# Kernel optimization log

Hardware: AMD Instinct MI355X
Metric: run time of the kernel (lower is better)

## Reference

```python
import jax, jax.numpy as jnp
import numpy as np

N, E, F_IN, F_OUT = 50000, 1600000, 256, 64
ALPHA = 0.2  # LeakyReLU negative slope


def setup_inputs() -> dict:
    key = jax.random.key(0)
    k1, k2, k3, k4 = jax.random.split(key, 4)
    x = jax.random.normal(k1, (N, F_IN), dtype=jnp.float32)
    edge = jax.random.randint(k2, (2, E), 0, N)  # COO (row, col) indices of adj
    # xavier_normal with gain=1.414 (as in the torch module)
    W = jax.random.normal(k3, (F_IN, F_OUT), dtype=jnp.float32) * (1.414 * np.sqrt(2.0 / (F_IN + F_OUT)))
    a = jax.random.normal(k4, (1, 2 * F_OUT), dtype=jnp.float32) * (1.414 * np.sqrt(2.0 / (1 + 2 * F_OUT)))
    return {"x": x, "edge": edge, "W": W, "a": a}


def reference(x, edge, W, a):
    # eval mode: dropout is a no-op
    Wh = x @ W  # [N, F_OUT]
    src, dst = edge[0], edge[1]
    # a @ concat(Wh[src], Wh[dst]) per edge, computed as two node-level dots then gathered
    s_src = Wh @ a[0, :F_OUT]   # [N]
    s_dst = Wh @ a[0, F_OUT:]   # [N]
    score = s_src[src] + s_dst[dst]                      # [E]
    edge_e = jnp.exp(-jax.nn.leaky_relu(score, ALPHA))   # [E]
    # sparse-softmax denominator: row sums of exp scores
    e_rowsum = jax.ops.segment_sum(edge_e, src, num_segments=N)  # [N]
    # weighted aggregation: h_prime[i] = sum_{(i,j) in E} e_ij * Wh[j]
    h_prime = jax.ops.segment_sum(edge_e[:, None] * Wh[dst], src, num_segments=N)  # [N, F_OUT]
    h_prime = h_prime / e_rowsum[:, None]
    return jax.nn.elu(h_prime)  # concat=True -> ELU
```

## Files before the change

### kernel.cpp

```cpp
#include <hip/hip_runtime.h>
#include <hip/hip_fp16.h>

#define N_NODES 50000
#define N_EDGES 1600000
#define F_IN 256
#define F_OUT 64
#define ALPHA 0.2f

#define BS 64
#define NBK 782
#define NSUB 8
#define CAP 384
#define EB 2048
#define NBB 782
#define LDS_CAP 4096
#define OF_CAP 16384

typedef __attribute__((ext_vector_type(8))) short bf16x8;
typedef __attribute__((ext_vector_type(4))) float f32x4;

__device__ inline unsigned short f2bf(float f) {
    unsigned int u = __float_as_uint(f);
    return (unsigned short)((u + 0x7FFFu + ((u >> 16) & 1u)) >> 16);
}
__device__ inline float bf2f(unsigned short b) {
    return __uint_as_float(((unsigned int)b) << 16);
}

__device__ inline void fmix_lo(float& a, unsigned int u, float s) {
    asm("v_fma_mix_f32 %0, %1, %2, %0 op_sel:[0,0,0] op_sel_hi:[1,0,0]"
        : "+v"(a) : "v"(u), "v"(s));
}
__device__ inline void fmix_hi(float& a, unsigned int u, float s) {
    asm("v_fma_mix_f32 %0, %1, %2, %0 op_sel:[1,0,0] op_sel_hi:[1,0,0]"
        : "+v"(a) : "v"(u), "v"(s));
}

__global__ __launch_bounds__(256) void gat_wprep(
    const float* __restrict__ W, unsigned short* __restrict__ Wf,
    int* __restrict__ cnt, int* __restrict__ of_cnt)
{
    const int di = blockIdx.x * 256 + threadIdx.x;
    if (di < NSUB * NBK) cnt[di] = 0;
    if (di == 0) of_cnt[0] = 0;
    const int j    = di & 7;
    const int lane = (di >> 3) & 63;
    const int tile = di >> 9;
    const int ks   = tile >> 2;
    const int nt   = tile & 3;
    const int k = ks * 32 + (lane >> 4) * 8 + j;
    const int n = nt * 16 + (lane & 15);
    Wf[di] = f2bf(W[k * F_OUT + n]);
}

__global__ __launch_bounds__(256) void gat_fused(
    const float* __restrict__ x, const unsigned short* __restrict__ Wf,
    const float* __restrict__ a, unsigned short* __restrict__ Whh,
    float* __restrict__ s_src, float* __restrict__ s_dst,
    const int* __restrict__ edge, int* __restrict__ cnt,
    unsigned int* __restrict__ arr, int* __restrict__ of_cnt,
    int2* __restrict__ of_list)
{
    __shared__ __align__(16) unsigned char smem[32768];
    const int t = threadIdx.x;

    if (blockIdx.x >= NBB) {
        unsigned short* Wl = (unsigned short*)smem;
        {
            const float4* __restrict__ src = (const float4*)Wf;
            float4* dst = (float4*)Wl;
            #pragma unroll
            for (int i = 0; i < 8; ++i) dst[t + i * 256] = src[t + i * 256];
        }
        __syncthreads();

        const int lane = t & 63;
        const int w    = t >> 6;
        const int q    = lane >> 4;
        const int c16  = lane & 15;
        const bf16x8* __restrict__ Wfrag = (const bf16x8*)Wl;

        float av[4], av2[4];
        #pragma unroll
        for (int nt = 0; nt < 4; ++nt) {
            av[nt]  = a[nt * 16 + c16];
            av2[nt] = a[F_OUT + nt * 16 + c16];
        }

        const int c = blockIdx.x - NBB;
        const int node0 = c * 64 + w * 16;
        int row = node0 + c16;
        if (row >= N_NODES) row = N_NODES - 1;
        const float4* __restrict__ xp = (const float4*)(x + (size_t)row * F_IN);

        float4 xv[16];
        #pragma unroll
        for (int ks = 0; ks < 8; ++ks) {
            xv[2 * ks]     = xp[ks * 8 + q * 2];
            xv[2 * ks + 1] = xp[ks * 8 + q * 2 + 1];
        }

        f32x4 acc[4];
        #pragma unroll
        for (int nt = 0; nt < 4; ++nt) acc[nt] = (f32x4){0.f, 0.f, 0.f, 0.f};

        #pragma unroll
        for (int ks = 0; ks < 8; ++ks) {
            float xf[8] = {xv[2*ks].x,   xv[2*ks].y,   xv[2*ks].z,   xv[2*ks].w,
                           xv[2*ks+1].x, xv[2*ks+1].y, xv[2*ks+1].z, xv[2*ks+1].w};
            bf16x8 ah, al;
            #pragma unroll
            for (int j = 0; j < 8; ++j) {
                const unsigned short h = f2bf(xf[j]);
                ah[j] = (short)h;
                al[j] = (short)f2bf(xf[j] - bf2f(h));
            }
            #pragma unroll
            for (int nt = 0; nt < 4; ++nt) {
                const bf16x8 bh = Wfrag[(ks * 4 + nt) * 64 + lane];
                acc[nt] = __builtin_amdgcn_mfma_f32_16x16x32_bf16(ah, bh, acc[nt], 0, 0, 0);
                acc[nt] = __builtin_amdgcn_mfma_f32_16x16x32_bf16(al, bh, acc[nt], 0, 0, 0);
            }
        }

        #pragma unroll
        for (int r = 0; r < 4; ++r) {
            const int node = node0 + q * 4 + r;
            float p = 0.f, qq = 0.f;
            #pragma unroll
            for (int nt = 0; nt < 4; ++nt) {
                const float v = acc[nt][r];
                if (node < N_NODES)
                    Whh[(size_t)node * F_OUT + nt * 16 + c16] =
                        __half_as_ushort(__float2half(v));
                p  = fmaf(v, av[nt], p);
                qq = fmaf(v, av2[nt], qq);
            }
            #pragma unroll
            for (int off = 1; off <= 8; off <<= 1) {
                p  += __shfl_xor(p, off);
                qq += __shfl_xor(qq, off);
            }
            if (c16 == 0 && node < N_NODES) { s_src[node] = p; s_dst[node] = qq; }
        }
    } else {
        int* lhist            = (int*)smem;
        int* lstart           = (int*)(smem + 3128);
        int* gbase            = (int*)(smem + 6260);
        int* cursor           = (int*)(smem + 9388);
        int* scanbuf          = (int*)(smem + 12516);
        unsigned int* sorted  = (unsigned int*)(smem + 13540);

        const int blk = blockIdx.x;
        const int e0  = blk * EB;
        const int sub = blk & 7;

        for (int i = t; i < NBK; i += 256) lhist[i] = 0;
        __syncthreads();

        int sreg[EB / 256];
        #pragma unroll
        for (int i = 0; i < EB / 256; ++i) {
            const int e = e0 + i * 256 + t;
            int s = -1;
            if (e < N_EDGES) {
                s = edge[e];
                atomicAdd(&lhist[s >> 6], 1);
            }
            sreg[i] = s;
        }
        __syncthreads();

        int psum = 0;
        {
            const int b0 = t * 4;
            #pragma unroll
            for (int i = 0; i < 4; ++i)
                if (b0 + i < NBK) psum += lhist[b0 + i];
        }
        scanbuf[t] = psum;
        __syncthreads();
        for (int off = 1; off < 256; off <<= 1) {
            const int v = (t >= off) ? scanbuf[t - off] : 0;
            __syncthreads();
            scanbuf[t] += v;
            __syncthreads();
        }
        {
            int run = scanbuf[t] - psum;
            const int b0 = t * 4;
            #pragma unroll
            for (int i = 0; i < 4; ++i) {
                const int b = b0 + i;
                if (b < NBK) {
                    lstart[b] = run;
                    cursor[b] = run;
                    run += lhist[b];
                }
            }
            if (t == 255) lstart[NBK] = scanbuf[255];
        }
        __syncthreads();

        for (int b = t; b < NBK; b += 256) {
            const int c = lhist[b];
            gbase[b] = (c > 0) ? atomicAdd(&cnt[sub * NBK + b], c) : 0;
        }

        #pragma unroll
        for (int i = 0; i < EB / 256; ++i) {
            const int s = sreg[i];
            if (s >= 0) {
                const int e = e0 + i * 256 + t;
                const int d = edge[N_EDGES + e];
                const int b = s >> 6;
                const int pos = atomicAdd(&cursor[b], 1);
                sorted[pos] = ((unsigned)b << 22) | ((unsigned)(s & 63) << 16) | (unsigned)d;
            }
        }
        __syncthreads();

        const int C = lstart[NBK];
        for (int p = t; p < C; p += 256) {
            const unsigned en = sorted[p];
            const int b = (int)(en >> 22);
            const int idx = gbase[b] + (p - lstart[b]);
            if (idx < CAP) {
                arr[((size_t)(sub * NBK + b)) * CAP + idx] = en & 0x3FFFFFu;
            } else {
                const int s = b * 64 + (int)((en >> 16) & 63);
                const int op = atomicAdd(of_cnt, 1);
                if (op < OF_CAP) of_list[op] = make_int2(s, (int)(en & 0xFFFFu));
            }
        }
    }
}

__global__ __launch_bounds__(512) void gat_aggregate(
    const int* __restrict__ cnt, const unsigned int* __restrict__ arr,
    const float* __restrict__ s_src, const float* __restrict__ s_dst,
    const unsigned short* __restrict__ Whh, const int* __restrict__ of_cnt,
    const int2* __restrict__ of_list, float* __restrict__ out)
{
    __shared__ uint2 ent2[LDS_CAP + 8];
    __shared__ int   bin[BS];
    __shared__ int   start[BS + 1];
    __shared__ int   Pl[NSUB + 1];
    const int t = threadIdx.x;
    const int lane = t & 63;
    const int w = t >> 6;
    const int b = blockIdx.x;

    if (t < BS) bin[t] = 0;
    if (t < 8) ent2[LDS_CAP + t] = make_uint2(0u, 0u);
    if (w == 0) {
        int c = (lane < NSUB) ? min(cnt[lane * NBK + b], CAP) : 0;
        int s = c;
        #pragma unroll
        for (int off = 1; off < NSUB; off <<= 1) {
            const int v = __shfl_up(s, off);
            if (lane >= off) s += v;
        }
        if (lane < NSUB) Pl[lane + 1] = s;
        if (lane == 0)   Pl[0] = 0;
    }
    __syncthreads();
    const int C = Pl[NSUB];
    const int nof = min(of_cnt[0], OF_CAP);

    unsigned enr[6];
    int nr = 0;
    for (int g = t; g < C; g += 512) {
        int sub = 0;
        #pragma unroll
        for (int s2 = 1; s2 < NSUB; ++s2) sub += (g >= Pl[s2]);
        const unsigned en = arr[((size_t)(sub * NBK + b)) * CAP + (g - Pl[sub])];
        enr[nr++] = en;
        atomicAdd(&bin[en >> 16], 1);
    }
    for (int i = t; i < nof; i += 512) {
        const int2 e2 = of_list[i];
        if ((e2.x >> 6) == b) atomicAdd(&bin[e2.x & 63], 1);
    }
    __syncthreads();
    if (w == 0) {
        const int c  = bin[lane];
        const int pc = (c + 7) & ~7;
        int s = pc;
        #pragma unroll
        for (int off = 1; off < BS; off <<= 1) {
            const int v = __shfl_up(s, off);
            if (lane >= off) s += v;
        }
        start[lane + 1] = s;
        if (lane == 0) start[0] = 0;
        bin[lane] = s - pc;
    }
    __syncthreads();

    for (int r = 0; r < nr; ++r) {
        const unsigned en = enr[r];
        const int sl = (int)(en >> 16);
        const int d  = (int)(en & 0xffffu);
        const float sc = s_src[b * BS + sl] + s_dst[d];
        const float ee = __expf(-(sc > 0.f ? sc : ALPHA * sc));
        const int pos = atomicAdd(&bin[sl], 1);
        if (pos < LDS_CAP) ent2[pos] = make_uint2((unsigned)d, __float_as_uint(ee));
    }
    for (int i = t; i < nof; i += 512) {
        const int2 e2 = of_list[i];
        if ((e2.x >> 6) == b) {
            const float sc = s_src[e2.x] + s_dst[e2.y];
            const float ee = __expf(-(sc > 0.f ? sc : ALPHA * sc));
            const int pos = atomicAdd(&bin[e2.x & 63], 1);
            if (pos < LDS_CAP) ent2[pos] = make_uint2((unsigned)e2.y, __float_as_uint(ee));
        }
    }
    __syncthreads();
    {
        const int n  = t & 63;
        const int e1 = min(start[n + 1], LDS_CAP);
        for (int p = bin[n] + (t >> 6); p < e1; p += 8)
            ent2[p] = make_uint2(0u, 0u);
    }
    __syncthreads();

    const int q  = lane >> 4;
    const int fq = lane & 15;
    const uint2* __restrict__ Whh2 = (const uint2*)Whh;

    #pragma unroll
    for (int nn = 0; nn < 2; ++nn) {
        const int n    = w * 8 + nn * 4 + q;
        const int node = b * BS + n;
        const int r0 = start[n];
        const int r1 = min(start[n + 1], LDS_CAP);
        float4 acc = make_float4(0.f, 0.f, 0.f, 0.f);
        float rsum = 0.f;
        for (int j = r0; j < r1; j += 8) {
            unsigned eu[8];
            uint2 wv[8];
            #pragma unroll
            for (int k = 0; k < 8; ++k) {
                const uint2 e = ent2[j + k];
                eu[k] = e.y;
                wv[k] = Whh2[(size_t)e.x * 16 + fq];
            }
            #pragma unroll
            for (int k = 0; k < 8; ++k) {
                const float et = __uint_as_float(eu[k]);
                fmix_lo(acc.x, wv[k].x, et);
                fmix_hi(acc.y, wv[k].x, et);
                fmix_lo(acc.z, wv[k].y, et);
                fmix_hi(acc.w, wv[k].y, et);
                rsum += et;
            }
        }
        const float rinv = __builtin_amdgcn_rcpf(rsum);
        float4 v;
        v.x = acc.x * rinv; v.y = acc.y * rinv;
        v.z = acc.z * rinv; v.w = acc.w * rinv;
        v.x = v.x > 0.f ? v.x : (__expf(v.x) - 1.f);
        v.y = v.y > 0.f ? v.y : (__expf(v.y) - 1.f);
        v.z = v.z > 0.f ? v.z : (__expf(v.z) - 1.f);
        v.w = v.w > 0.f ? v.w : (__expf(v.w) - 1.f);
        if (node < N_NODES)
            ((float4*)out)[(size_t)node * 16 + fq] = v;
    }
}

extern "C" void kernel_launch(void* const* d_in, const int* in_sizes, int n_in,
                              void* d_out, int out_size, void* d_ws, size_t ws_size,
                              hipStream_t stream) {
    const float* x    = (const float*)d_in[0];
    const int*   edge = (const int*)  d_in[1];
    const float* W    = (const float*)d_in[2];
    const float* a    = (const float*)d_in[3];
    float* out = (float*)d_out;

    unsigned short* Whh   = (unsigned short*)d_ws;
    unsigned int*   arr   = (unsigned int*)(Whh + (size_t)N_NODES * F_OUT);
    float*          s_src = (float*)(arr + (size_t)NSUB * NBK * CAP);
    float*          s_dst = s_src + N_NODES;
    int*            cnt   = (int*)(s_dst + N_NODES);
    int2*           of_list = (int2*)(cnt + NSUB * NBK);
    int*            of_cnt  = (int*)(of_list + OF_CAP);
    unsigned short* Wf      = (unsigned short*)(of_cnt + 4);

    gat_wprep<<<64, 256, 0, stream>>>(W, Wf, cnt, of_cnt);
    gat_fused<<<NBB + NBK, 256, 0, stream>>>(x, Wf, a, Whh, s_src, s_dst,
                                             edge, cnt, arr, of_cnt, of_list);
    gat_aggregate<<<NBK, 512, 0, stream>>>(cnt, arr, s_src, s_dst, Whh,
                                           of_cnt, of_list, out);
}
```

Measured before the change: 151.7 us.

## Pack LDS edge entries into 32 bits and gather Wh rows with 16-byte loads

Each edge entry in LDS is now packed into one 32-bit word: the 16-bit destination index in the high half and the bf16-rounded edge weight in the low half. LDS_CAP also shrinks, which cuts LDS use per block and should allow more resident blocks. The aggregation loop now assigns 8 lanes per node, each loading 16 bytes of Wh, so a wave covers 8 nodes in one pass instead of two passes of 4 nodes with 8-byte loads. In exchange the edge weights lose precision to bf16, both in the numerator and in the row sum. The smaller cap also raises the chance that very high-degree blocks overflow LDS.

```diff
diff --git a/kernel.cpp b/kernel.cpp
--- a/kernel.cpp
+++ b/kernel.cpp
@@ -13,7 +13,7 @@
 #define CAP 384
 #define EB 2048
 #define NBB 782
-#define LDS_CAP 4096
+#define LDS_CAP 3584
 #define OF_CAP 16384
 
 typedef __attribute__((ext_vector_type(8))) short bf16x8;
@@ -242,17 +242,17 @@
     const unsigned short* __restrict__ Whh, const int* __restrict__ of_cnt,
     const int2* __restrict__ of_list, float* __restrict__ out)
 {
-    __shared__ uint2 ent2[LDS_CAP + 8];
-    __shared__ int   bin[BS];
-    __shared__ int   start[BS + 1];
-    __shared__ int   Pl[NSUB + 1];
+    __shared__ unsigned int ent2[LDS_CAP + 8];
+    __shared__ int bin[BS];
+    __shared__ int start[BS + 1];
+    __shared__ int Pl[NSUB + 1];
     const int t = threadIdx.x;
     const int lane = t & 63;
     const int w = t >> 6;
     const int b = blockIdx.x;
 
     if (t < BS) bin[t] = 0;
-    if (t < 8) ent2[LDS_CAP + t] = make_uint2(0u, 0u);
+    if (t < 8) ent2[LDS_CAP + t] = 0u;
     if (w == 0) {
         int c = (lane < NSUB) ? min(cnt[lane * NBK + b], CAP) : 0;
         int s = c;
@@ -305,7 +305,7 @@
         const float sc = s_src[b * BS + sl] + s_dst[d];
         const float ee = __expf(-(sc > 0.f ? sc : ALPHA * sc));
         const int pos = atomicAdd(&bin[sl], 1);
-        if (pos < LDS_CAP) ent2[pos] = make_uint2((unsigned)d, __float_as_uint(ee));
+        if (pos < LDS_CAP) ent2[pos] = ((unsigned)d << 16) | (unsigned)f2bf(ee);
     }
     for (int i = t; i < nof; i += 512) {
         const int2 e2 = of_list[i];
@@ -313,7 +313,7 @@
             const float sc = s_src[e2.x] + s_dst[e2.y];
             const float ee = __expf(-(sc > 0.f ? sc : ALPHA * sc));
             const int pos = atomicAdd(&bin[e2.x & 63], 1);
-            if (pos < LDS_CAP) ent2[pos] = make_uint2((unsigned)e2.y, __float_as_uint(ee));
+            if (pos < LDS_CAP) ent2[pos] = ((unsigned)e2.y << 16) | (unsigned)f2bf(ee);
         }
     }
     __syncthreads();
@@ -321,51 +321,59 @@
         const int n  = t & 63;
         const int e1 = min(start[n + 1], LDS_CAP);
         for (int p = bin[n] + (t >> 6); p < e1; p += 8)
-            ent2[p] = make_uint2(0u, 0u);
+            ent2[p] = 0u;
     }
     __syncthreads();
 
-    const int q  = lane >> 4;
-    const int fq = lane & 15;
-    const uint2* __restrict__ Whh2 = (const uint2*)Whh;
-
-    #pragma unroll
-    for (int nn = 0; nn < 2; ++nn) {
-        const int n    = w * 8 + nn * 4 + q;
-        const int node = b * BS + n;
-        const int r0 = start[n];
-        const int r1 = min(start[n + 1], LDS_CAP);
-        float4 acc = make_float4(0.f, 0.f, 0.f, 0.f);
-        float rsum = 0.f;
-        for (int j = r0; j < r1; j += 8) {
-            unsigned eu[8];
-            uint2 wv[8];
-            #pragma unroll
-            for (int k = 0; k < 8; ++k) {
-                const uint2 e = ent2[j + k];
-                eu[k] = e.y;
-                wv[k] = Whh2[(size_t)e.x * 16 + fq];
-            }
-            #pragma unroll
-            for (int k = 0; k < 8; ++k) {
-                const float et = __uint_as_float(eu[k]);
-                fmix_lo(acc.x, wv[k].x, et);
-                fmix_hi(acc.y, wv[k].x, et);
-                fmix_lo(acc.z, wv[k].y, et);
-                fmix_hi(acc.w, wv[k].y, et);
-                rsum += et;
-            }
-        }
-        const float rinv = __builtin_amdgcn_rcpf(rsum);
-        float4 v;
-        v.x = acc.x * rinv; v.y = acc.y * rinv;
-        v.z = acc.z * rinv; v.w = acc.w * rinv;
-        v.x = v.x > 0.f ? v.x : (__expf(v.x) - 1.f);
-        v.y = v.y > 0.f ? v.y : (__expf(v.y) - 1.f);
-        v.z = v.z > 0.f ? v.z : (__expf(v.z) - 1.f);
-        v.w = v.w > 0.f ? v.w : (__expf(v.w) - 1.f);
-        if (node < N_NODES)
-            ((float4*)out)[(size_t)node * 16 + fq] = v;
+    const int q8 = lane >> 3;
+    const int f8 = lane & 7;
+    const uint4* __restrict__ Whh4 = (const uint4*)Whh;
+
+    const int n    = w * 8 + q8;
+    const int node = b * BS + n;
+    const int r0 = start[n];
+    const int r1 = min(start[n + 1], LDS_CAP);
+    float4 a0 = make_float4(0.f, 0.f, 0.f, 0.f);
+    float4 a1 = make_float4(0.f, 0.f, 0.f, 0.f);
+    float rsum = 0.f;
+    for (int j = r0; j < r1; j += 8) {
+        unsigned eu[8];
+        uint4 wv[8];
+        #pragma unroll
+        for (int k = 0; k < 8; ++k) {
+            const unsigned e = ent2[j + k];
+            eu[k] = e;
+            wv[k] = Whh4[(size_t)(e >> 16) * 8 + f8];
+        }
+        #pragma unroll
+        for (int k = 0; k < 8; ++k) {
+            const float et = __uint_as_float(eu[k] << 16);
+            fmix_lo(a0.x, wv[k].x, et);
+            fmix_hi(a0.y, wv[k].x, et);
+            fmix_lo(a0.z, wv[k].y, et);
+            fmix_hi(a0.w, wv[k].y, et);
+            fmix_lo(a1.x, wv[k].z, et);
+            fmix_hi(a1.y, wv[k].z, et);
+            fmix_lo(a1.z, wv[k].w, et);
+            fmix_hi(a1.w, wv[k].w, et);
+            rsum += et;
+        }
+    }
+    const float rinv = __builtin_amdgcn_rcpf(rsum);
+    float4 v0, v1;
+    v0.x = a0.x * rinv; v0.y = a0.y * rinv; v0.z = a0.z * rinv; v0.w = a0.w * rinv;
+    v1.x = a1.x * rinv; v1.y = a1.y * rinv; v1.z = a1.z * rinv; v1.w = a1.w * rinv;
+    v0.x = v0.x > 0.f ? v0.x : (__expf(v0.x) - 1.f);
+    v0.y = v0.y > 0.f ? v0.y : (__expf(v0.y) - 1.f);
+    v0.z = v0.z > 0.f ? v0.z : (__expf(v0.z) - 1.f);
+    v0.w = v0.w > 0.f ? v0.w : (__expf(v0.w) - 1.f);
+    v1.x = v1.x > 0.f ? v1.x : (__expf(v1.x) - 1.f);
+    v1.y = v1.y > 0.f ? v1.y : (__expf(v1.y) - 1.f);
+    v1.z = v1.z > 0.f ? v1.z : (__expf(v1.z) - 1.f);
+    v1.w = v1.w > 0.f ? v1.w : (__expf(v1.w) - 1.f);
+    if (node < N_NODES) {
+        ((float4*)out)[(size_t)node * 16 + f8 * 2]     = v0;
+        ((float4*)out)[(size_t)node * 16 + f8 * 2 + 1] = v1;
     }
 }
 
```

After: 148.3 us. -2.2%, faster.
